# Kernel optimization log

Hardware: AMD Instinct MI355X
Metric: run time of the kernel (lower is better)

## Reference

```python
import jax, jax.numpy as jnp
import numpy as np
import math

E_LENGTH = 64


def setup_inputs() -> dict:
    key = jax.random.key(0)
    ks = jax.random.split(key, 9)
    B, L, D, N, H = 4, 1024, 1024, 16, 64
    scale = 0.05  # emulate xavier-normal scale
    return {
        "x": jax.random.normal(ks[0], (B, L, D), dtype=jnp.float32),
        "mask": jnp.ones((B, L), dtype=jnp.int32),
        "w_q": jax.random.normal(ks[1], (N, D, H), dtype=jnp.float32) * scale,
        "w_k": jax.random.normal(ks[2], (N, D, H), dtype=jnp.float32) * scale,
        "w_v": jax.random.normal(ks[3], (N, D, H), dtype=jnp.float32) * scale,
        "w_o": jax.random.normal(ks[4], (N, H, D), dtype=jnp.float32) * scale,
        "q_embed_table": jax.random.normal(ks[5], (2 * E_LENGTH - 1, H), dtype=jnp.float32) * scale,
        "k_embed_table": jax.random.normal(ks[6], (2 * E_LENGTH - 1, H), dtype=jnp.float32) * scale,
        "v_embed_table": jax.random.normal(ks[7], (2 * E_LENGTH - 1, H), dtype=jnp.float32) * scale,
    }


def reference(x, mask, w_q, w_k, w_v, w_o, q_embed_table, k_embed_table, v_embed_table):
    # x: [B, L, d_model], mask: [B, L]
    L = x.shape[1]
    d_qkv = w_q.shape[-1]
    e = E_LENGTH

    q = jnp.einsum('blm,nmh->bnlh', x, w_q)
    k = jnp.einsum('blm,nmh->bnlh', x, w_k)
    v = jnp.einsum('blm,nmh->bnlh', x, w_v)

    pos = jnp.arange(L)
    # clipped relative distance indices in [0, 2e-2]
    dist = jnp.clip(pos[:, None] - pos[None, :], -(e - 1), e - 1) + (e - 1)  # [L, L]

    scores = jnp.einsum('bnid,bnjd->bnij', q, k)
    # mode contains 'q': key-side bias uses k_embedding
    k_embed = k_embed_table[dist]  # [L, L, d]
    scores = scores + jnp.einsum('bnjd,ijd->bnij', k, k_embed)
    # mode contains 'k': query-side bias uses q_embedding
    q_embed = q_embed_table[dist]  # [L, L, d]
    scores = scores + jnp.einsum('bnid,ijd->bnij', q, q_embed)

    scores = scores / math.sqrt(d_qkv)
    scores = jnp.where((mask == 0)[:, None, None, :], jnp.float32(-1e9), scores)
    p_attn = jax.nn.softmax(scores, axis=-1)  # [B, N, L, L]

    out = jnp.einsum('bnij,bnjd->bnid', p_attn, v)
    # mode contains 'v': value-side relative bias
    v_embed = v_embed_table[dist]  # [L, L, d]
    out = out + jnp.einsum('bnij,ijd->bnid', p_attn, v_embed)

    # per-head output projection, then sum over heads
    return jnp.einsum('bnid,ndm->bim', out, w_o)
```

## Files before the change

kernel.cpp:

```cpp
#include <hip/hip_runtime.h>


typedef __bf16 bf16x8 __attribute__((ext_vector_type(8)));
typedef float f32x4 __attribute__((ext_vector_type(4)));
typedef unsigned int u32x4 __attribute__((ext_vector_type(4)));

__device__ __forceinline__ unsigned short f2bf(float f) {
    unsigned int u = __builtin_bit_cast(unsigned int, f);
    u += 0x7fffu + ((u >> 16) & 1u);
    return (unsigned short)(u >> 16);
}
__device__ __forceinline__ float bf2f(unsigned short s) {
    unsigned int u = ((unsigned int)s) << 16;
    return __builtin_bit_cast(float, u);
}

__device__ __forceinline__ void gl2lds16(const unsigned short* g, unsigned short* l) {
    __builtin_amdgcn_global_load_lds(
        (const __attribute__((address_space(1))) unsigned int*)g,
        (__attribute__((address_space(3))) unsigned int*)l, 16, 0, 0);
}

__global__ void convert_kernel(const float* __restrict__ x,
                               const float* __restrict__ wq,
                               const float* __restrict__ wk,
                               const float* __restrict__ wv,
                               const float* __restrict__ wo,
                               const float* __restrict__ qe,
                               const float* __restrict__ ke,
                               const float* __restrict__ ve,
                               unsigned short* __restrict__ x_bf,
                               unsigned short* __restrict__ wqkv_bt,
                               unsigned short* __restrict__ wo_bt,
                               unsigned short* __restrict__ qe_bf,
                               unsigned short* __restrict__ ke_bf,
                               unsigned short* __restrict__ ve_t)
{
    const size_t R0 = 4u * 1024 * 1024;
    const size_t R1 = R0 + 3u * 1024 * 1024;
    const size_t R2 = R1 + 1024u * 1024;
    const size_t R3 = R2 + 8192;
    const size_t R4 = R3 + 8192;
    const size_t R5 = R4 + 8192;
    size_t stride = (size_t)gridDim.x * blockDim.x;
    for (size_t i = (size_t)blockIdx.x * blockDim.x + threadIdx.x; i < R5; i += stride) {
        if (i < R0) {
            x_bf[i] = f2bf(x[i]);
        } else if (i < R1) {
            size_t j = i - R0;
            int which = (int)(j >> 20);
            int rem = (int)(j & 0xFFFFF);
            int n = rem >> 16, d = (rem >> 6) & 1023, h = rem & 63;
            const float* w = which == 0 ? wq : which == 1 ? wk : wv;
            wqkv_bt[(size_t)(which * 1024 + n * 64 + h) * 1024 + d] = f2bf(w[rem]);
        } else if (i < R2) {
            int rem = (int)(i - R1);
            int n = rem >> 16, h = (rem >> 10) & 63, m = rem & 1023;
            wo_bt[(size_t)m * 1024 + n * 64 + h] = f2bf(wo[rem]);
        } else if (i < R3) {
            int idx = (int)(i - R2);
            int e = idx >> 6;
            qe_bf[idx] = (e < 127) ? f2bf(qe[idx]) : 0;
        } else if (i < R4) {
            int idx = (int)(i - R3);
            int e = idx >> 6;
            ke_bf[idx] = (e < 127) ? f2bf(ke[idx]) : 0;
        } else {
            int idx = (int)(i - R4);
            int h = idx >> 7, e = idx & 127;
            ve_t[idx] = (e < 127) ? f2bf(ve[e * 64 + h]) : 0;
        }
    }
}

template<int MODE>
__global__ __launch_bounds__(256) void gemm_bt_kernel(
    const unsigned short* __restrict__ A,
    const unsigned short* __restrict__ Bt,
    int K, int lda, int ldb,
    void* __restrict__ C0, void* __restrict__ C1, void* __restrict__ C2,
    int ldc)
{
    __shared__ unsigned short As[128 * 64];
    __shared__ unsigned short Bs[128 * 64];
    const int m0 = blockIdx.y * 128;
    const int n0 = blockIdx.x * 128;
    const int tid = threadIdx.x;
    const int lane = tid & 63;
    const int w = tid >> 6;
    const int wr = w >> 1, wc = w & 1;
    const int g = lane >> 4, c16 = lane & 15;

    f32x4 acc[4][4];
#pragma unroll
    for (int i = 0; i < 4; ++i)
#pragma unroll
        for (int j = 0; j < 4; ++j) acc[i][j] = f32x4{0.f, 0.f, 0.f, 0.f};

    for (int kt = 0; kt < K; kt += 64) {
#pragma unroll
        for (int c = 0; c < 4; ++c) {
            int chunk = c * 256 + tid;
            int row = chunk >> 3, col = (chunk & 7) * 8;
            unsigned short* ldsA = &As[(c * 256 + w * 64) * 8];
            unsigned short* ldsB = &Bs[(c * 256 + w * 64) * 8];
            gl2lds16(A  + (size_t)(m0 + row) * lda + kt + col, ldsA);
            gl2lds16(Bt + (size_t)(n0 + row) * ldb + kt + col, ldsB);
        }
        __syncthreads();
#pragma unroll
        for (int ks = 0; ks < 2; ++ks) {
            bf16x8 af[4], bfr[4];
#pragma unroll
            for (int mi = 0; mi < 4; ++mi)
                af[mi] = __builtin_bit_cast(bf16x8,
                    *reinterpret_cast<const u32x4*>(&As[(wr * 64 + mi * 16 + c16) * 64 + ks * 32 + g * 8]));
#pragma unroll
            for (int ni = 0; ni < 4; ++ni)
                bfr[ni] = __builtin_bit_cast(bf16x8,
                    *reinterpret_cast<const u32x4*>(&Bs[(wc * 64 + ni * 16 + c16) * 64 + ks * 32 + g * 8]));
#pragma unroll
            for (int mi = 0; mi < 4; ++mi)
#pragma unroll
                for (int ni = 0; ni < 4; ++ni)
                    acc[mi][ni] = __builtin_amdgcn_mfma_f32_16x16x32_bf16(af[mi], bfr[ni], acc[mi][ni], 0, 0, 0);
        }
        __syncthreads();
    }

#pragma unroll
    for (int mi = 0; mi < 4; ++mi) {
#pragma unroll
        for (int ni = 0; ni < 4; ++ni) {
#pragma unroll
            for (int r = 0; r < 4; ++r) {
                int m = m0 + wr * 64 + mi * 16 + g * 4 + r;
                int c = n0 + wc * 64 + ni * 16 + c16;
                float v = acc[mi][ni][r];
                if (MODE == 0) {
                    int b = m >> 10, l = m & 1023;
                    int which = c >> 10, n = (c >> 6) & 15, h = c & 63;
                    if (which == 2) {
                        ((unsigned short*)C2)[(((size_t)b * 16 + n) * 64 + h) * 1024 + l] = f2bf(v);
                    } else {
                        unsigned short* dst = (unsigned short*)(which == 0 ? C0 : C1);
                        dst[(((size_t)b * 16 + n) * 1024 + l) * 64 + h] = f2bf(v);
                    }
                }
            }
        }
    }
}

__global__ __launch_bounds__(256) void proj_kernel(
    const unsigned short* __restrict__ q_buf,
    const unsigned short* __restrict__ k_buf,
    const unsigned short* __restrict__ qe_bf,
    const unsigned short* __restrict__ ke_bf,
    unsigned short* __restrict__ q_proj,
    unsigned short* __restrict__ k_proj,
    unsigned short* __restrict__ kp_edge)
{
    __shared__ unsigned short As[128 * 64];
    __shared__ unsigned short Bs[128 * 64];
    const int by = blockIdx.y;
    const int which = by >> 9;
    const int m0 = (by & 511) * 128;
    const unsigned short* A  = which ? k_buf : q_buf;
    const unsigned short* Bt = which ? ke_bf : qe_bf;
    unsigned short* C0 = which ? k_proj : q_proj;

    const int tid = threadIdx.x;
    const int lane = tid & 63;
    const int w = tid >> 6;
    const int wr = w >> 1, wc = w & 1;
    const int g = lane >> 4, c16 = lane & 15;

    f32x4 acc[4][4];
#pragma unroll
    for (int i = 0; i < 4; ++i)
#pragma unroll
        for (int j = 0; j < 4; ++j) acc[i][j] = f32x4{0.f, 0.f, 0.f, 0.f};

#pragma unroll
    for (int c = 0; c < 4; ++c) {
        int chunk = c * 256 + tid;
        int row = chunk >> 3, col = (chunk & 7) * 8;
        unsigned short* ldsA = &As[(c * 256 + w * 64) * 8];
        unsigned short* ldsB = &Bs[(c * 256 + w * 64) * 8];
        gl2lds16(A  + (size_t)(m0 + row) * 64 + col, ldsA);
        gl2lds16(Bt + (size_t)row * 64 + col, ldsB);
    }
    __syncthreads();
#pragma unroll
    for (int ks = 0; ks < 2; ++ks) {
        bf16x8 af[4], bfr[4];
#pragma unroll
        for (int mi = 0; mi < 4; ++mi)
            af[mi] = __builtin_bit_cast(bf16x8,
                *reinterpret_cast<const u32x4*>(&As[(wr * 64 + mi * 16 + c16) * 64 + ks * 32 + g * 8]));
#pragma unroll
        for (int ni = 0; ni < 4; ++ni)
            bfr[ni] = __builtin_bit_cast(bf16x8,
                *reinterpret_cast<const u32x4*>(&Bs[(wc * 64 + ni * 16 + c16) * 64 + ks * 32 + g * 8]));
#pragma unroll
        for (int mi = 0; mi < 4; ++mi)
#pragma unroll
            for (int ni = 0; ni < 4; ++ni)
                acc[mi][ni] = __builtin_amdgcn_mfma_f32_16x16x32_bf16(af[mi], bfr[ni], acc[mi][ni], 0, 0, 0);
    }

#pragma unroll
    for (int mi = 0; mi < 4; ++mi) {
#pragma unroll
        for (int ni = 0; ni < 4; ++ni) {
#pragma unroll
            for (int r = 0; r < 4; ++r) {
                int m = m0 + wr * 64 + mi * 16 + g * 4 + r;
                int c = wc * 64 + ni * 16 + c16;
                float v = acc[mi][ni][r];
                C0[(size_t)m * 128 + c] = f2bf(v);
                if (which && (c == 0 || c == 126))
                    kp_edge[(size_t)(c ? 65536 : 0) + m] = f2bf(v);
            }
        }
    }
}

__global__ __launch_bounds__(256) void gemm_n64_kernel(
    const unsigned short* __restrict__ A,
    const unsigned short* __restrict__ Bt,
    float* __restrict__ C)
{
    __shared__ unsigned short As[128 * 64];
    __shared__ unsigned short Bs[64 * 64];
    const int m0 = blockIdx.y * 128;
    const int n0 = blockIdx.x * 64;
    const int tid = threadIdx.x;
    const int lane = tid & 63;
    const int w = tid >> 6;
    const int g = lane >> 4, c16 = lane & 15;

    f32x4 acc[2][4];
#pragma unroll
    for (int i = 0; i < 2; ++i)
#pragma unroll
        for (int j = 0; j < 4; ++j) acc[i][j] = f32x4{0.f, 0.f, 0.f, 0.f};

    for (int kt = 0; kt < 1024; kt += 64) {
#pragma unroll
        for (int c = 0; c < 4; ++c) {
            int chunk = c * 256 + tid;
            int row = chunk >> 3, col = (chunk & 7) * 8;
            unsigned short* ldsA = &As[(c * 256 + w * 64) * 8];
            gl2lds16(A + (size_t)(m0 + row) * 1024 + kt + col, ldsA);
        }
#pragma unroll
        for (int c = 0; c < 2; ++c) {
            int chunk = c * 256 + tid;
            int row = chunk >> 3, col = (chunk & 7) * 8;
            unsigned short* ldsB = &Bs[(c * 256 + w * 64) * 8];
            gl2lds16(Bt + (size_t)(n0 + row) * 1024 + kt + col, ldsB);
        }
        __syncthreads();
#pragma unroll
        for (int ks = 0; ks < 2; ++ks) {
            bf16x8 af[2], bfr[4];
#pragma unroll
            for (int mi = 0; mi < 2; ++mi)
                af[mi] = __builtin_bit_cast(bf16x8,
                    *reinterpret_cast<const u32x4*>(&As[(w * 32 + mi * 16 + c16) * 64 + ks * 32 + g * 8]));
#pragma unroll
            for (int ni = 0; ni < 4; ++ni)
                bfr[ni] = __builtin_bit_cast(bf16x8,
                    *reinterpret_cast<const u32x4*>(&Bs[(ni * 16 + c16) * 64 + ks * 32 + g * 8]));
#pragma unroll
            for (int mi = 0; mi < 2; ++mi)
#pragma unroll
                for (int ni = 0; ni < 4; ++ni)
                    acc[mi][ni] = __builtin_amdgcn_mfma_f32_16x16x32_bf16(af[mi], bfr[ni], acc[mi][ni], 0, 0, 0);
        }
        __syncthreads();
    }

#pragma unroll
    for (int mi = 0; mi < 2; ++mi)
#pragma unroll
        for (int ni = 0; ni < 4; ++ni)
#pragma unroll
            for (int r = 0; r < 4; ++r) {
                int m = m0 + w * 32 + mi * 16 + g * 4 + r;
                int cc = n0 + ni * 16 + c16;
                C[(size_t)m * 1024 + cc] = acc[mi][ni][r];
            }
}

#define ATTN_LDS_BYTES 54784

__global__ __launch_bounds__(512, 4) void attn_kernel(
    const unsigned short* __restrict__ q_buf,
    const unsigned short* __restrict__ k_buf,
    const unsigned short* __restrict__ v_t,
    const unsigned short* __restrict__ q_proj,
    const unsigned short* __restrict__ k_proj,
    const unsigned short* __restrict__ kp_edge,
    const unsigned short* __restrict__ ve_t,
    const int* __restrict__ mask,
    unsigned short* __restrict__ attn_out)
{
    extern __shared__ char smem[];
    unsigned short* Ks = (unsigned short*)smem;
    unsigned short* Vt = (unsigned short*)(smem + 9216);
    unsigned short* Ps = (unsigned short*)(smem + 18432);
    unsigned short* kp = (unsigned short*)(smem + 36864);
    float* mj   = (float*)(smem + 54272);
    float* kpej = (float*)(smem + 54528);
    unsigned short* veT = (unsigned short*)smem;
    unsigned short* peB = (unsigned short*)(smem + 17408);
    float* lrow = (float*)(smem + 52224);

    const int id = blockIdx.x;
    const int bn = id & 63;
    const int ib = id >> 6;
    const int b = bn >> 4;
    const int i0 = ib * 128;
    const int tid = threadIdx.x;
    const int lane = tid & 63;
    const int w = tid >> 6;
    const int g = lane >> 4, c16 = lane & 15;
    const int il = tid >> 2;
    const int part = tid & 3;

    const int jlo = 2 * ib - 1, jhi = 2 * ib + 2;

    const int sr = tid >> 3,  sc = (tid & 7) * 8;

    bf16x8 qf[2];
    {
        const unsigned short* qrow = q_buf + ((size_t)bn * 1024 + i0 + w * 16 + c16) * 64;
        qf[0] = __builtin_bit_cast(bf16x8, *reinterpret_cast<const u32x4*>(qrow + g * 8));
        qf[1] = __builtin_bit_cast(bf16x8, *reinterpret_cast<const u32x4*>(qrow + 32 + g * 8));
    }
    f32x4 qp0v, qp126v;
#pragma unroll
    for (int r = 0; r < 4; ++r) {
        size_t row = (size_t)bn * 1024 + i0 + w * 16 + g * 4 + r;
        qp0v[r]   = 0.125f * bf2f(q_proj[row * 128 + 0]);
        qp126v[r] = 0.125f * bf2f(q_proj[row * 128 + 126]);
    }

    float peR[32];
#pragma unroll
    for (int k = 0; k < 32; ++k) peR[k] = 0.f;
    float lreg = 0.f, acc0 = 0.f, acc126 = 0.f;
    f32x4 accO[4];
#pragma unroll
    for (int i = 0; i < 4; ++i) accO[i] = f32x4{0.f, 0.f, 0.f, 0.f};

    for (int jt = 0; jt < 16; ++jt) {
        const int j0 = jt * 64;
        const bool need_kp = (jt >= jlo) && (jt <= jhi);

        {
            u32x4 kv = *reinterpret_cast<const u32x4*>(k_buf + ((size_t)bn * 1024 + j0 + sr) * 64 + sc);
            u32x4 vv = *reinterpret_cast<const u32x4*>(v_t + ((size_t)bn * 64 + sr) * 1024 + j0 + sc);
            *reinterpret_cast<u32x4*>(&Ks[sr * 72 + sc]) = kv;
            *reinterpret_cast<u32x4*>(&Vt[sr * 72 + sc]) = vv;
        }
        if (need_kp) {
#pragma unroll
            for (int c = 0; c < 2; ++c) {
                int chunk = tid + c * 512;
                int row = chunk >> 4, col = (chunk & 15) * 8;
                u32x4 v = *reinterpret_cast<const u32x4*>(k_proj + ((size_t)bn * 1024 + j0 + row) * 128 + col);
                *reinterpret_cast<u32x4*>(&kp[row * 136 + col]) = v;
            }
        }
        if (tid < 64) {
            mj[tid] = mask[b * 1024 + j0 + tid] ? 1.f : 0.f;
            kpej[tid] = 0.125f * bf2f(kp_edge[(size_t)(jt < 2 * ib ? 65536 : 0) + bn * 1024 + j0 + tid]);
        }
        __syncthreads();

        f32x4 sacc[4];
#pragma unroll
        for (int nf = 0; nf < 4; ++nf) sacc[nf] = f32x4{0.f, 0.f, 0.f, 0.f};
#pragma unroll
        for (int ks = 0; ks < 2; ++ks)
#pragma unroll
            for (int nf = 0; nf < 4; ++nf) {
                bf16x8 kf = __builtin_bit_cast(bf16x8,
                    *reinterpret_cast<const u32x4*>(&Ks[(nf * 16 + c16) * 72 + ks * 32 + g * 8]));
                sacc[nf] = __builtin_amdgcn_mfma_f32_16x16x32_bf16(qf[ks], kf, sacc[nf], 0, 0, 0);
            }

        const int dw = i0 + w * 16 - j0;
        if (dw < 126 && dw > -78) {
            const int d0 = i0 - j0 + 63;
            const unsigned short* qpg = q_proj + ((size_t)bn * 1024 + i0) * 128;
#pragma unroll
            for (int nf = 0; nf < 4; ++nf) {
                int j_l = nf * 16 + c16;
                float mfl = mj[j_l];
#pragma unroll
                for (int r = 0; r < 4; ++r) {
                    int i_l = w * 16 + g * 4 + r;
                    int e = d0 + i_l - j_l;
                    e = e < 0 ? 0 : (e > 126 ? 126 : e);
                    float s = sacc[nf][r] + bf2f(kp[j_l * 136 + e]) + bf2f(qpg[i_l * 128 + e]);
                    s *= 0.125f;
                    float p = (mfl > 0.f) ? __expf(s) : 0.f;
                    Ps[i_l * 72 + j_l] = f2bf(p);
                }
            }
        } else {
            const f32x4 qpc = (dw >= 126) ? qp126v : qp0v;
#pragma unroll
            for (int nf = 0; nf < 4; ++nf) {
                int j_l = nf * 16 + c16;
                float kv = kpej[j_l];
                float mfl = mj[j_l];
#pragma unroll
                for (int r = 0; r < 4; ++r) {
                    float s = sacc[nf][r] * 0.125f + kv + qpc[r];
                    float p = (mfl > 0.f) ? __expf(s) : 0.f;
                    Ps[(w * 16 + g * 4 + r) * 72 + j_l] = f2bf(p);
                }
            }
        }

#pragma unroll
        for (int ks = 0; ks < 2; ++ks) {
            bf16x8 pf = __builtin_bit_cast(bf16x8,
                *reinterpret_cast<const u32x4*>(&Ps[(w * 16 + c16) * 72 + ks * 32 + g * 8]));
#pragma unroll
            for (int nf2 = 0; nf2 < 4; ++nf2) {
                bf16x8 vf = __builtin_bit_cast(bf16x8,
                    *reinterpret_cast<const u32x4*>(&Vt[(nf2 * 16 + c16) * 72 + ks * 32 + g * 8]));
                accO[nf2] = __builtin_amdgcn_mfma_f32_16x16x32_bf16(pf, vf, accO[nf2], 0, 0, 0);
            }
        }

        {
            bf16x8 s0 = __builtin_bit_cast(bf16x8,
                *reinterpret_cast<const u32x4*>(&Ps[il * 72 + part * 16]));
            bf16x8 s1 = __builtin_bit_cast(bf16x8,
                *reinterpret_cast<const u32x4*>(&Ps[il * 72 + part * 16 + 8]));
            float v[16];
#pragma unroll
            for (int m = 0; m < 8; ++m) { v[m] = (float)s0[m]; v[8 + m] = (float)s1[m]; }
            float rs = 0.f;
#pragma unroll
            for (int m = 0; m < 16; ++m) rs += v[m];
            rs += __shfl_xor(rs, 1);
            rs += __shfl_xor(rs, 2);
            lreg += rs;

            const int base = i0 + il - j0 + 63;
            if (base >= 189) {
                acc126 += rs;
            } else if (base <= 0) {
                acc0 += rs;
            } else {
                float b0 = 0.f, b126 = 0.f;
#pragma unroll
                for (int m = 0; m < 16; ++m) {
                    int jl = part * 16 + m;
                    if (jl >= base) b0 += v[m];
                    if (jl <= base - 126) b126 += v[m];
                }
                b0 += __shfl_xor(b0, 1);     b0 += __shfl_xor(b0, 2);
                b126 += __shfl_xor(b126, 1); b126 += __shfl_xor(b126, 2);
                if (part == 0) peR[0] += b0;
                if (part == 3) peR[30] += b126;
#pragma unroll
                for (int k = 0; k < 32; ++k) {
                    int e = part * 32 + k;
                    int jl = base - e;
                    if (e >= 1 && e <= 125 && jl >= 0 && jl < 64)
                        peR[k] += bf2f(Ps[il * 72 + jl]);
                }
            }
        }
        __syncthreads();
    }

    if (part == 0) peR[0] += acc0;
    if (part == 3) peR[30] += acc126;

#pragma unroll
    for (int c = 0; c < 2; ++c) {
        int chunk = tid + c * 512;
        int h = chunk >> 4, col = (chunk & 15) * 8;
        u32x4 vv = *reinterpret_cast<const u32x4*>(ve_t + h * 128 + col);
        *reinterpret_cast<u32x4*>(&veT[h * 136 + col]) = vv;
    }
#pragma unroll
    for (int kk = 0; kk < 4; ++kk) {
        bf16x8 pk;
#pragma unroll
        for (int e2 = 0; e2 < 8; ++e2) pk[e2] = (__bf16)peR[kk * 8 + e2];
        *reinterpret_cast<u32x4*>(&peB[il * 136 + part * 32 + kk * 8]) =
            __builtin_bit_cast(u32x4, pk);
    }
    if (part == 0) lrow[il] = lreg;
    __syncthreads();

#pragma unroll
    for (int ks = 0; ks < 4; ++ks) {
        bf16x8 pf = __builtin_bit_cast(bf16x8,
            *reinterpret_cast<const u32x4*>(&peB[(w * 16 + c16) * 136 + ks * 32 + g * 8]));
#pragma unroll
        for (int nf2 = 0; nf2 < 4; ++nf2) {
            bf16x8 vf = __builtin_bit_cast(bf16x8,
                *reinterpret_cast<const u32x4*>(&veT[(nf2 * 16 + c16) * 136 + ks * 32 + g * 8]));
            accO[nf2] = __builtin_amdgcn_mfma_f32_16x16x32_bf16(pf, vf, accO[nf2], 0, 0, 0);
        }
    }

#pragma unroll
    for (int nf2 = 0; nf2 < 4; ++nf2) {
#pragma unroll
        for (int r = 0; r < 4; ++r) {
            int i_l = w * 16 + g * 4 + r;
            int h = nf2 * 16 + c16;
            float vv = accO[nf2][r] / lrow[i_l];
            attn_out[(((size_t)b * 1024 + i0 + i_l) * 16 + (bn & 15)) * 64 + h] = f2bf(vv);
        }
    }
}

extern "C" void kernel_launch(void* const* d_in, const int* in_sizes, int n_in,
                              void* d_out, int out_size, void* d_ws, size_t ws_size,
                              hipStream_t stream)
{
    const float* x  = (const float*)d_in[0];
    const int* mask = (const int*)d_in[1];
    const float* wq = (const float*)d_in[2];
    const float* wk = (const float*)d_in[3];
    const float* wv = (const float*)d_in[4];
    const float* wo = (const float*)d_in[5];
    const float* qe = (const float*)d_in[6];
    const float* ke = (const float*)d_in[7];
    const float* ve = (const float*)d_in[8];

    char* ws = (char*)d_ws;
    size_t off = 0;
    auto carve = [&](size_t bytes) -> char* {
        char* p = ws + off;
        off += (bytes + 255) & ~(size_t)255;
        return p;
    };
    unsigned short* x_bf    = (unsigned short*)carve(4096ull * 1024 * 2);
    unsigned short* wqkv_bt = (unsigned short*)carve(3072ull * 1024 * 2);
    unsigned short* wo_bt   = (unsigned short*)carve(1024ull * 1024 * 2);
    unsigned short* qe_bf   = (unsigned short*)carve(128ull * 64 * 2);
    unsigned short* ke_bf   = (unsigned short*)carve(128ull * 64 * 2);
    unsigned short* ve_t    = (unsigned short*)carve(64ull * 128 * 2);
    unsigned short* q_buf   = (unsigned short*)carve(65536ull * 64 * 2);
    unsigned short* k_buf   = (unsigned short*)carve(65536ull * 64 * 2);
    unsigned short* v_t     = (unsigned short*)carve(65536ull * 64 * 2);
    unsigned short* q_proj  = (unsigned short*)carve(65536ull * 128 * 2);
    unsigned short* k_proj  = (unsigned short*)carve(65536ull * 128 * 2);
    unsigned short* kp_edge = (unsigned short*)carve(2ull * 65536 * 2);
    unsigned short* attn_o  = x_bf;
    (void)ws_size; (void)in_sizes; (void)n_in; (void)out_size;

    convert_kernel<<<2048, 256, 0, stream>>>(x, wq, wk, wv, wo, qe, ke, ve,
                                             x_bf, wqkv_bt, wo_bt, qe_bf, ke_bf, ve_t);

    gemm_bt_kernel<0><<<dim3(24, 32), 256, 0, stream>>>(
        x_bf, wqkv_bt, 1024, 1024, 1024, q_buf, k_buf, v_t, 0);

    proj_kernel<<<dim3(1, 1024), 256, 0, stream>>>(
        q_buf, k_buf, qe_bf, ke_bf, q_proj, k_proj, kp_edge);

    hipFuncSetAttribute((const void*)attn_kernel,
                        hipFuncAttributeMaxDynamicSharedMemorySize, ATTN_LDS_BYTES);
    attn_kernel<<<512, 512, ATTN_LDS_BYTES, stream>>>(
        q_buf, k_buf, v_t, q_proj, k_proj, kp_edge, ve_t, mask, attn_o);

    gemm_n64_kernel<<<dim3(16, 32), 256, 0, stream>>>(attn_o, wo_bt, (float*)d_out);
}
```

Before: 218.5 us.

## Tile weight transposes through LDS and coalesce V-transpose stores in QKV GEMM

The fp32-to-bf16 conversion kernel moves from a grid-stride scalar loop with strided transposed writes to per-block tiles. x is converted with vector loads and stores, and the weight transposes go through a padded LDS tile so both reads and writes are coalesced. The QKV GEMM epilogue for the V columns now stages the accumulators in swizzled LDS and writes 16-byte coalesced rows of v_t, replacing scattered 2-byte stores with a stride of 1024. This targets uncoalesced global writes in the preprocessing and projection stages, at the cost of an extra LDS round trip and a barrier.

```diff
diff --git a/kernel.cpp b/kernel.cpp
--- a/kernel.cpp
+++ b/kernel.cpp
@@ -4,6 +4,7 @@
 typedef __bf16 bf16x8 __attribute__((ext_vector_type(8)));
 typedef float f32x4 __attribute__((ext_vector_type(4)));
 typedef unsigned int u32x4 __attribute__((ext_vector_type(4)));
+typedef unsigned short u16x4 __attribute__((ext_vector_type(4)));
 
 __device__ __forceinline__ unsigned short f2bf(float f) {
     unsigned int u = __builtin_bit_cast(unsigned int, f);
@@ -21,68 +22,100 @@
         (__attribute__((address_space(3))) unsigned int*)l, 16, 0, 0);
 }
 
-__global__ void convert_kernel(const float* __restrict__ x,
-                               const float* __restrict__ wq,
-                               const float* __restrict__ wk,
-                               const float* __restrict__ wv,
-                               const float* __restrict__ wo,
-                               const float* __restrict__ qe,
-                               const float* __restrict__ ke,
-                               const float* __restrict__ ve,
-                               unsigned short* __restrict__ x_bf,
-                               unsigned short* __restrict__ wqkv_bt,
-                               unsigned short* __restrict__ wo_bt,
-                               unsigned short* __restrict__ qe_bf,
-                               unsigned short* __restrict__ ke_bf,
-                               unsigned short* __restrict__ ve_t)
+__global__ __launch_bounds__(256) void convert_kernel(
+    const float* __restrict__ x,
+    const float* __restrict__ wq,
+    const float* __restrict__ wk,
+    const float* __restrict__ wv,
+    const float* __restrict__ wo,
+    const float* __restrict__ qe,
+    const float* __restrict__ ke,
+    const float* __restrict__ ve,
+    unsigned short* __restrict__ x_bf,
+    unsigned short* __restrict__ wqkv_bt,
+    unsigned short* __restrict__ wo_bt,
+    unsigned short* __restrict__ qe_bf,
+    unsigned short* __restrict__ ke_bf,
+    unsigned short* __restrict__ ve_t)
 {
-    const size_t R0 = 4u * 1024 * 1024;
-    const size_t R1 = R0 + 3u * 1024 * 1024;
-    const size_t R2 = R1 + 1024u * 1024;
-    const size_t R3 = R2 + 8192;
-    const size_t R4 = R3 + 8192;
-    const size_t R5 = R4 + 8192;
-    size_t stride = (size_t)gridDim.x * blockDim.x;
-    for (size_t i = (size_t)blockIdx.x * blockDim.x + threadIdx.x; i < R5; i += stride) {
-        if (i < R0) {
-            x_bf[i] = f2bf(x[i]);
-        } else if (i < R1) {
-            size_t j = i - R0;
-            int which = (int)(j >> 20);
-            int rem = (int)(j & 0xFFFFF);
-            int n = rem >> 16, d = (rem >> 6) & 1023, h = rem & 63;
-            const float* w = which == 0 ? wq : which == 1 ? wk : wv;
-            wqkv_bt[(size_t)(which * 1024 + n * 64 + h) * 1024 + d] = f2bf(w[rem]);
-        } else if (i < R2) {
-            int rem = (int)(i - R1);
-            int n = rem >> 16, h = (rem >> 10) & 63, m = rem & 1023;
-            wo_bt[(size_t)m * 1024 + n * 64 + h] = f2bf(wo[rem]);
-        } else if (i < R3) {
-            int idx = (int)(i - R2);
-            int e = idx >> 6;
-            qe_bf[idx] = (e < 127) ? f2bf(qe[idx]) : 0;
-        } else if (i < R4) {
-            int idx = (int)(i - R3);
-            int e = idx >> 6;
-            ke_bf[idx] = (e < 127) ? f2bf(ke[idx]) : 0;
-        } else {
-            int idx = (int)(i - R4);
-            int h = idx >> 7, e = idx & 127;
-            ve_t[idx] = (e < 127) ? f2bf(ve[e * 64 + h]) : 0;
-        }
-    }
-}
-
-template<int MODE>
-__global__ __launch_bounds__(256) void gemm_bt_kernel(
+    __shared__ unsigned short T[64 * 72];
+    const int bid = blockIdx.x;
+    const int tid = threadIdx.x;
+
+    if (bid < 512) {
+        const float* src = x + (size_t)bid * 8192;
+        unsigned short* dst = x_bf + (size_t)bid * 8192;
+#pragma unroll
+        for (int c = 0; c < 8; ++c) {
+            int idx = c * 1024 + tid * 4;
+            f32x4 v = *reinterpret_cast<const f32x4*>(src + idx);
+            u16x4 o = u16x4{f2bf(v[0]), f2bf(v[1]), f2bf(v[2]), f2bf(v[3])};
+            *reinterpret_cast<u16x4*>(dst + idx) = o;
+        }
+    } else if (bid < 1280) {
+        int t = bid - 512;
+        int which = t >> 8, n = (t >> 4) & 15, dt = t & 15;
+        const float* w = which == 0 ? wq : which == 1 ? wk : wv;
+        const float* src = w + ((size_t)n * 1024 + dt * 64) * 64;
+#pragma unroll
+        for (int c = 0; c < 4; ++c) {
+            int chunk = c * 256 + tid;
+            int dd = chunk >> 4, hh = (chunk & 15) * 4;
+            f32x4 v = *reinterpret_cast<const f32x4*>(src + dd * 64 + hh);
+#pragma unroll
+            for (int j = 0; j < 4; ++j) T[(hh + j) * 72 + dd] = f2bf(v[j]);
+        }
+        __syncthreads();
+        unsigned short* dstb = wqkv_bt + ((size_t)(which * 1024 + n * 64)) * 1024 + dt * 64;
+#pragma unroll
+        for (int c = 0; c < 2; ++c) {
+            int chunk = c * 256 + tid;
+            int h = chunk >> 3, d8 = (chunk & 7) * 8;
+            u32x4 v = *reinterpret_cast<const u32x4*>(&T[h * 72 + d8]);
+            *reinterpret_cast<u32x4*>(dstb + (size_t)h * 1024 + d8) = v;
+        }
+    } else if (bid < 1536) {
+        int t = bid - 1280;
+        int n = t >> 4, mt = t & 15;
+        const float* src = wo + (size_t)n * 64 * 1024 + mt * 64;
+#pragma unroll
+        for (int c = 0; c < 4; ++c) {
+            int chunk = c * 256 + tid;
+            int hh = chunk >> 4, mm = (chunk & 15) * 4;
+            f32x4 v = *reinterpret_cast<const f32x4*>(src + (size_t)hh * 1024 + mm);
+#pragma unroll
+            for (int j = 0; j < 4; ++j) T[(mm + j) * 72 + hh] = f2bf(v[j]);
+        }
+        __syncthreads();
+        unsigned short* dstb = wo_bt + (size_t)(mt * 64) * 1024 + n * 64;
+#pragma unroll
+        for (int c = 0; c < 2; ++c) {
+            int chunk = c * 256 + tid;
+            int m = chunk >> 3, h8 = (chunk & 7) * 8;
+            u32x4 v = *reinterpret_cast<const u32x4*>(&T[m * 72 + h8]);
+            *reinterpret_cast<u32x4*>(dstb + (size_t)m * 1024 + h8) = v;
+        }
+    } else {
+        for (int i = tid; i < 8192; i += 256) {
+            int e = i >> 6;
+            qe_bf[i] = (e < 127) ? f2bf(qe[i]) : 0;
+            ke_bf[i] = (e < 127) ? f2bf(ke[i]) : 0;
+            int h = i >> 7, e2 = i & 127;
+            ve_t[i] = (e2 < 127) ? f2bf(ve[e2 * 64 + h]) : 0;
+        }
+    }
+}
+
+__global__ __launch_bounds__(256) void gemm_qkv_kernel(
     const unsigned short* __restrict__ A,
     const unsigned short* __restrict__ Bt,
-    int K, int lda, int ldb,
-    void* __restrict__ C0, void* __restrict__ C1, void* __restrict__ C2,
-    int ldc)
+    unsigned short* __restrict__ q_buf,
+    unsigned short* __restrict__ k_buf,
+    unsigned short* __restrict__ v_t)
 {
-    __shared__ unsigned short As[128 * 64];
-    __shared__ unsigned short Bs[128 * 64];
+    __shared__ unsigned short Sh[2 * 128 * 64];
+    unsigned short* As = Sh;
+    unsigned short* Bs = Sh + 8192;
     const int m0 = blockIdx.y * 128;
     const int n0 = blockIdx.x * 128;
     const int tid = threadIdx.x;
@@ -97,15 +130,15 @@
 #pragma unroll
         for (int j = 0; j < 4; ++j) acc[i][j] = f32x4{0.f, 0.f, 0.f, 0.f};
 
-    for (int kt = 0; kt < K; kt += 64) {
+    for (int kt = 0; kt < 1024; kt += 64) {
 #pragma unroll
         for (int c = 0; c < 4; ++c) {
             int chunk = c * 256 + tid;
             int row = chunk >> 3, col = (chunk & 7) * 8;
             unsigned short* ldsA = &As[(c * 256 + w * 64) * 8];
             unsigned short* ldsB = &Bs[(c * 256 + w * 64) * 8];
-            gl2lds16(A  + (size_t)(m0 + row) * lda + kt + col, ldsA);
-            gl2lds16(Bt + (size_t)(n0 + row) * ldb + kt + col, ldsB);
+            gl2lds16(A  + (size_t)(m0 + row) * 1024 + kt + col, ldsA);
+            gl2lds16(Bt + (size_t)(n0 + row) * 1024 + kt + col, ldsB);
         }
         __syncthreads();
 #pragma unroll
@@ -128,26 +161,41 @@
         __syncthreads();
     }
 
-#pragma unroll
-    for (int mi = 0; mi < 4; ++mi) {
-#pragma unroll
-        for (int ni = 0; ni < 4; ++ni) {
-#pragma unroll
-            for (int r = 0; r < 4; ++r) {
-                int m = m0 + wr * 64 + mi * 16 + g * 4 + r;
-                int c = n0 + wc * 64 + ni * 16 + c16;
-                float v = acc[mi][ni][r];
-                if (MODE == 0) {
+    if (n0 < 2048) {
+#pragma unroll
+        for (int mi = 0; mi < 4; ++mi)
+#pragma unroll
+            for (int ni = 0; ni < 4; ++ni)
+#pragma unroll
+                for (int r = 0; r < 4; ++r) {
+                    int m = m0 + wr * 64 + mi * 16 + g * 4 + r;
+                    int c = n0 + wc * 64 + ni * 16 + c16;
                     int b = m >> 10, l = m & 1023;
                     int which = c >> 10, n = (c >> 6) & 15, h = c & 63;
-                    if (which == 2) {
-                        ((unsigned short*)C2)[(((size_t)b * 16 + n) * 64 + h) * 1024 + l] = f2bf(v);
-                    } else {
-                        unsigned short* dst = (unsigned short*)(which == 0 ? C0 : C1);
-                        dst[(((size_t)b * 16 + n) * 1024 + l) * 64 + h] = f2bf(v);
-                    }
+                    unsigned short* dst = which == 0 ? q_buf : k_buf;
+                    dst[(((size_t)b * 16 + n) * 1024 + l) * 64 + h] = f2bf(acc[mi][ni][r]);
                 }
-            }
+    } else {
+#pragma unroll
+        for (int mi = 0; mi < 4; ++mi)
+#pragma unroll
+            for (int ni = 0; ni < 4; ++ni)
+#pragma unroll
+                for (int r = 0; r < 4; ++r) {
+                    int l = wr * 64 + mi * 16 + g * 4 + r;
+                    int cr = wc * 64 + ni * 16 + c16;
+                    Sh[cr * 128 + (l ^ ((cr & 7) << 3))] = f2bf(acc[mi][ni][r]);
+                }
+        __syncthreads();
+        const int b = m0 >> 10;
+        const size_t rowbase = (size_t)(b * 1024 + (n0 - 2048)) * 1024 + (m0 & 1023);
+#pragma unroll
+        for (int c = 0; c < 8; ++c) {
+            int chunk = c * 256 + tid;
+            int cr = chunk >> 4, l0 = (chunk & 15) * 8;
+            int lsw = l0 ^ ((cr & 7) << 3);
+            u32x4 vv = *reinterpret_cast<const u32x4*>(&Sh[cr * 128 + lsw]);
+            *reinterpret_cast<u32x4*>(v_t + rowbase + (size_t)cr * 1024 + l0) = vv;
         }
     }
 }
@@ -566,11 +614,11 @@
     unsigned short* attn_o  = x_bf;
     (void)ws_size; (void)in_sizes; (void)n_in; (void)out_size;
 
-    convert_kernel<<<2048, 256, 0, stream>>>(x, wq, wk, wv, wo, qe, ke, ve,
+    convert_kernel<<<1537, 256, 0, stream>>>(x, wq, wk, wv, wo, qe, ke, ve,
                                              x_bf, wqkv_bt, wo_bt, qe_bf, ke_bf, ve_t);
 
-    gemm_bt_kernel<0><<<dim3(24, 32), 256, 0, stream>>>(
-        x_bf, wqkv_bt, 1024, 1024, 1024, q_buf, k_buf, v_t, 0);
+    gemm_qkv_kernel<<<dim3(24, 32), 256, 0, stream>>>(
+        x_bf, wqkv_bt, q_buf, k_buf, v_t);
 
     proj_kernel<<<dim3(1, 1024), 256, 0, stream>>>(
         q_buf, k_buf, qe_bf, ke_bf, q_proj, k_proj, kp_edge);
```

After: 192.8 us. 1.13x faster.
